# Performance work log

Measured on AMD Instinct MI355X. Metric: run time of the kernel, lower is better.

The kernel has to match this reference:

```python
import jax, jax.numpy as jnp
import numpy as np

B, N, D = 16, 32768, 256
OUT = 256
TOP_K = 64


def setup_inputs() -> dict:
    key = jax.random.key(0)
    ks = jax.random.split(key, 10)
    s = 0.02
    return {
        "tem_emb": jax.random.normal(ks[0], (B, N, D), dtype=jnp.float32),
        "year": 1,
        "init_hidden": jax.random.normal(ks[1], (D, 1), dtype=jnp.float32) * s,
        "mlp_w": jax.random.normal(ks[2], (OUT, TOP_K * D), dtype=jnp.float32) * s,
        "mlp_b": jnp.zeros((OUT,), dtype=jnp.float32),
        "Wr_w": jax.random.normal(ks[3], (OUT, 2 * OUT), dtype=jnp.float32) * s,
        "Wr_b": jnp.zeros((OUT,), dtype=jnp.float32),
        "Wz_w": jax.random.normal(ks[4], (OUT, 2 * OUT), dtype=jnp.float32) * s,
        "Wz_b": jnp.zeros((OUT,), dtype=jnp.float32),
        "Wt_w": jax.random.normal(ks[5], (OUT, 2 * OUT), dtype=jnp.float32) * s,
        "Wt_b": jnp.zeros((OUT,), dtype=jnp.float32),
    }


def reference(tem_emb, year, init_hidden, mlp_w, mlp_b, Wr_w, Wr_b, Wz_w, Wz_b, Wt_w, Wt_b):
    b, n, d = tem_emb.shape
    x = jnp.swapaxes(tem_emb, 1, 2)              # [B, D, N]
    h0 = init_hidden[:, 0]                        # [D]; no prev year -> init_hidden branch
    prev = h0[None, :, None]                      # broadcasts to [B, D, N]

    # select_k=True: abs-diff top-k over N, per (B, D) row
    diff = jnp.abs(x - prev)                      # [B, D, N]
    _, top_idx = jax.lax.top_k(diff, TOP_K)       # [B, D, K]
    feats = jnp.take_along_axis(x, top_idx, axis=2)  # [B, D, K]
    flat = feats.reshape(b, d * TOP_K)            # [B, D*K]
    ts_in = flat @ mlp_w.T + mlp_b                # [B, OUT]

    # is_update=True: GatedUpdateCell(ts_in, mean_N(prev_hidden))
    h_prev = jnp.broadcast_to(h0, (b, d))         # mean over N of constant broadcast
    comb = jnp.concatenate([ts_in, h_prev], axis=-1)          # [B, 2*OUT]
    r = jax.nn.sigmoid(comb @ Wr_w.T + Wr_b)
    z = jax.nn.sigmoid(comb @ Wz_w.T + Wz_b)
    comb2 = jnp.concatenate([ts_in, h_prev * r], axis=-1)
    h_t = jnp.tanh(comb2 @ Wt_w.T + Wt_b)
    h_next = z * h_t + (1.0 - z) * ts_in          # [B, OUT]

    return jnp.broadcast_to(h_next[:, :, None], (b, OUT, n))  # [B, OUT, N]
```

## Files before the change

### kernel.cpp

```cpp
#include <hip/hip_runtime.h>
#include <stdint.h>

#define BB 16
#define NN 32768
#define DD 256
#define OUTD 256
#define TOPK 64
#define NTASK (BB * DD)
#define THRESH 2.75f
#define CAPMAX 512

typedef unsigned long long u64;
typedef unsigned int u32;

__device__ __forceinline__ u64 make_key(float diff, int n) {
    union { float f; u32 i; } c; c.f = diff;
    return ((u64)c.i << 15) | (u64)(u32)(32767 - n);
}

__global__ __launch_bounds__(256) void k_scan(const float4* __restrict__ t4,
                                              const float* __restrict__ h0,
                                              u32* __restrict__ cnt,
                                              u64* __restrict__ surv,
                                              int cap) {
    __shared__ float h0s[DD];
    h0s[threadIdx.x] = h0[threadIdx.x];
    __syncthreads();
    const int total = (BB * NN * DD) / 4;
    for (int v = blockIdx.x * blockDim.x + threadIdx.x; v < total; v += gridDim.x * blockDim.x) {
        float4 w = t4[v];
        int d0 = (v & 63) << 2;
        int n  = (v >> 6) & (NN - 1);
        int b  = v >> 21;
        float xs[4] = {w.x, w.y, w.z, w.w};
#pragma unroll
        for (int q = 0; q < 4; ++q) {
            float df = fabsf(xs[q] - h0s[d0 + q]);
            if (df >= THRESH) {
                int task = (b << 8) + d0 + q;
                u32 pos = atomicAdd(&cnt[task], 1u);
                if ((int)pos < cap)
                    surv[(size_t)task * cap + pos] = make_key(df, n);
            }
        }
    }
}

__global__ __launch_bounds__(64) void k_select(const u32* __restrict__ cnt,
                                               const u64* __restrict__ surv,
                                               const float* __restrict__ tem,
                                               float* __restrict__ feats, int cap) {
    int task = blockIdx.x;
    int c = (int)cnt[task];
    if (c < TOPK || c > cap) return;
    __shared__ u64 keys[CAPMAX];
    for (int i = threadIdx.x; i < CAPMAX; i += 64)
        keys[i] = (i < c) ? surv[(size_t)task * cap + i] : 0ull;
    __syncthreads();
    for (int k = 2; k <= CAPMAX; k <<= 1) {
        for (int j = k >> 1; j > 0; j >>= 1) {
            for (int i = threadIdx.x; i < CAPMAX; i += 64) {
                int ixj = i ^ j;
                if (ixj > i) {
                    u64 a = keys[i], bb = keys[ixj];
                    bool up = ((i & k) == 0);
                    if (up ? (a < bb) : (a > bb)) { keys[i] = bb; keys[ixj] = a; }
                }
            }
            __syncthreads();
        }
    }
    if (threadIdx.x < TOPK) {
        int n = 32767 - (int)(keys[threadIdx.x] & 0x7FFFu);
        int b = task >> 8, d = task & 255;
        feats[task * TOPK + threadIdx.x] = tem[((size_t)b * NN + n) * DD + d];
    }
}

__global__ __launch_bounds__(64) void k_fallback(const float* __restrict__ tem,
                                                 const float* __restrict__ h0,
                                                 const u32* __restrict__ cnt,
                                                 float* __restrict__ feats, int cap) {
    int task = blockIdx.x;
    int c = (int)cnt[task];
    if (c >= TOPK && c <= cap) return;
    int b = task >> 8, d = task & 255;
    float h = h0[d];
    int lane = threadIdx.x;
    const float* base = tem + (size_t)b * NN * DD + d;
    u64 prev = ~0ull;
    for (int k = 0; k < TOPK; ++k) {
        u64 best = 0ull;
        for (int n = lane; n < NN; n += 64) {
            float df = fabsf(base[(size_t)n * DD] - h);
            u64 key = make_key(df, n);
            if (key < prev && key > best) best = key;
        }
        for (int off = 32; off > 0; off >>= 1) {
            u64 o = __shfl_xor(best, off, 64);
            if (o > best) best = o;
        }
        if (lane == 0) {
            int n = 32767 - (int)(best & 0x7FFFu);
            feats[task * TOPK + k] = base[(size_t)n * DD];
        }
        prev = best;
    }
}

__global__ __launch_bounds__(256) void k_mlp(const float* __restrict__ mlp_w,
                                             const float* __restrict__ feats,
                                             float* __restrict__ ts_raw) {
    int Wv = blockIdx.x * 4 + (threadIdx.x >> 6);
    int lane = threadIdx.x & 63;
    int o = Wv >> 4, b = Wv & 15;
    const float4* w4 = (const float4*)(mlp_w + (size_t)o * (DD * TOPK));
    const float4* f4 = (const float4*)(feats + b * (DD * TOPK));
    float acc = 0.f;
    for (int j = lane; j < (DD * TOPK) / 4; j += 64) {
        float4 wv = w4[j]; float4 fv = f4[j];
        acc += wv.x * fv.x + wv.y * fv.y + wv.z * fv.z + wv.w * fv.w;
    }
    for (int off = 32; off > 0; off >>= 1) acc += __shfl_down(acc, off, 64);
    if (lane == 0) ts_raw[b * OUTD + o] = acc;
}

__global__ __launch_bounds__(256) void k_gru(const float* __restrict__ ts_raw,
                                             const float* __restrict__ mlp_b,
                                             const float* __restrict__ h0,
                                             const float* __restrict__ Wr_w,
                                             const float* __restrict__ Wr_b,
                                             const float* __restrict__ Wz_w,
                                             const float* __restrict__ Wz_b,
                                             const float* __restrict__ Wt_w,
                                             const float* __restrict__ Wt_b,
                                             float* __restrict__ h_next) {
    int b = blockIdx.x, o = threadIdx.x;
    __shared__ float comb[2 * OUTD];
    __shared__ float rh[OUTD];
    float ts = ts_raw[b * OUTD + o] + mlp_b[o];
    float h = h0[o];
    comb[o] = ts; comb[OUTD + o] = h;
    __syncthreads();
    const float4* wr = (const float4*)(Wr_w + (size_t)o * 2 * OUTD);
    const float4* wz = (const float4*)(Wz_w + (size_t)o * 2 * OUTD);
    float ar = Wr_b[o], az = Wz_b[o];
    for (int j = 0; j < (2 * OUTD) / 4; ++j) {
        float4 a = wr[j];
        ar += a.x * comb[4 * j] + a.y * comb[4 * j + 1] + a.z * comb[4 * j + 2] + a.w * comb[4 * j + 3];
        float4 c = wz[j];
        az += c.x * comb[4 * j] + c.y * comb[4 * j + 1] + c.z * comb[4 * j + 2] + c.w * comb[4 * j + 3];
    }
    float r = 1.f / (1.f + expf(-ar));
    float z = 1.f / (1.f + expf(-az));
    rh[o] = h * r;
    __syncthreads();
    const float4* wt = (const float4*)(Wt_w + (size_t)o * 2 * OUTD);
    float at = Wt_b[o];
    for (int j = 0; j < OUTD / 4; ++j) {
        float4 a = wt[j];
        at += a.x * comb[4 * j] + a.y * comb[4 * j + 1] + a.z * comb[4 * j + 2] + a.w * comb[4 * j + 3];
    }
    for (int j = 0; j < OUTD / 4; ++j) {
        float4 a = wt[OUTD / 4 + j];
        at += a.x * rh[4 * j] + a.y * rh[4 * j + 1] + a.z * rh[4 * j + 2] + a.w * rh[4 * j + 3];
    }
    float ht = tanhf(at);
    h_next[b * OUTD + o] = z * ht + (1.f - z) * ts;
}

__global__ __launch_bounds__(256) void k_bcast(const float* __restrict__ h_next,
                                               float4* __restrict__ out) {
    const int total = (BB * OUTD * NN) / 4;
    for (int v = blockIdx.x * blockDim.x + threadIdx.x; v < total; v += gridDim.x * blockDim.x) {
        int row = v >> 13;
        float h = h_next[row];
        out[v] = make_float4(h, h, h, h);
    }
}

extern "C" void kernel_launch(void* const* d_in, const int* in_sizes, int n_in,
                              void* d_out, int out_size, void* d_ws, size_t ws_size,
                              hipStream_t stream) {
    const float* tem   = (const float*)d_in[0];
    const float* h0    = (const float*)d_in[2];
    const float* mlp_w = (const float*)d_in[3];
    const float* mlp_b = (const float*)d_in[4];
    const float* Wr_w  = (const float*)d_in[5];
    const float* Wr_b  = (const float*)d_in[6];
    const float* Wz_w  = (const float*)d_in[7];
    const float* Wz_b  = (const float*)d_in[8];
    const float* Wt_w  = (const float*)d_in[9];
    const float* Wt_b  = (const float*)d_in[10];

    char* ws = (char*)d_ws;
    u32* cnt      = (u32*)ws;
    float* ts_raw = (float*)(ws + 16384);
    float* h_next = (float*)(ws + 32768);
    float* feats  = (float*)(ws + 49152);
    const size_t surv_off = 49152 + 1048576;
    u64* surv = (u64*)(ws + surv_off);
    int cap = 0;
    if (ws_size > surv_off) {
        size_t avail = (ws_size - surv_off) / ((size_t)NTASK * 8);
        cap = (int)(avail > CAPMAX ? CAPMAX : avail);
    }

    hipMemsetAsync(cnt, 0, NTASK * sizeof(u32), stream);
    k_scan<<<8192, 256, 0, stream>>>((const float4*)tem, h0, cnt, surv, cap);
    k_select<<<NTASK, 64, 0, stream>>>(cnt, surv, tem, feats, cap);
    k_fallback<<<NTASK, 64, 0, stream>>>(tem, h0, cnt, feats, cap);
    k_mlp<<<1024, 256, 0, stream>>>(mlp_w, feats, ts_raw);
    k_gru<<<BB, 256, 0, stream>>>(ts_raw, mlp_b, h0, Wr_w, Wr_b, Wz_w, Wz_b, Wt_w, Wt_b, h_next);
    k_bcast<<<8192, 256, 0, stream>>>(h_next, (float4*)d_out);
}
```

Measured before the change: 1.094 ms.

## Replace bitonic sort with rank counting, merge fallback, share MLP weight loads

```diff
diff --git a/kernel.cpp b/kernel.cpp
--- a/kernel.cpp
+++ b/kernel.cpp
@@ -46,83 +46,81 @@
     }
 }
 
-__global__ __launch_bounds__(64) void k_select(const u32* __restrict__ cnt,
-                                               const u64* __restrict__ surv,
-                                               const float* __restrict__ tem,
-                                               float* __restrict__ feats, int cap) {
+__global__ __launch_bounds__(128) void k_select(const u32* __restrict__ cnt,
+                                                const u64* __restrict__ surv,
+                                                const float* __restrict__ tem,
+                                                const float* __restrict__ h0,
+                                                float* __restrict__ feats, int cap) {
     int task = blockIdx.x;
     int c = (int)cnt[task];
-    if (c < TOPK || c > cap) return;
-    __shared__ u64 keys[CAPMAX];
-    for (int i = threadIdx.x; i < CAPMAX; i += 64)
-        keys[i] = (i < c) ? surv[(size_t)task * cap + i] : 0ull;
-    __syncthreads();
-    for (int k = 2; k <= CAPMAX; k <<= 1) {
-        for (int j = k >> 1; j > 0; j >>= 1) {
-            for (int i = threadIdx.x; i < CAPMAX; i += 64) {
-                int ixj = i ^ j;
-                if (ixj > i) {
-                    u64 a = keys[i], bb = keys[ixj];
-                    bool up = ((i & k) == 0);
-                    if (up ? (a < bb) : (a > bb)) { keys[i] = bb; keys[ixj] = a; }
-                }
-            }
-            __syncthreads();
+    int b = task >> 8, d = task & 255;
+    if (c >= TOPK && c <= cap) {
+        __shared__ u64 keys[CAPMAX];
+        for (int i = threadIdx.x; i < c; i += 128)
+            keys[i] = surv[(size_t)task * cap + i];
+        __syncthreads();
+        for (int i = threadIdx.x; i < c; i += 128) {
+            u64 me = keys[i];
+            int rank = 0;
+#pragma unroll 4
+            for (int j = 0; j < c; ++j)
+                rank += (keys[j] > me) ? 1 : 0;
+            if (rank < TOPK) {
+                int n = 32767 - (int)(me & 0x7FFFu);
+                feats[task * TOPK + rank] = tem[((size_t)b * NN + n) * DD + d];
+            }
         }
-    }
-    if (threadIdx.x < TOPK) {
-        int n = 32767 - (int)(keys[threadIdx.x] & 0x7FFFu);
-        int b = task >> 8, d = task & 255;
-        feats[task * TOPK + threadIdx.x] = tem[((size_t)b * NN + n) * DD + d];
-    }
-}
-
-__global__ __launch_bounds__(64) void k_fallback(const float* __restrict__ tem,
-                                                 const float* __restrict__ h0,
-                                                 const u32* __restrict__ cnt,
-                                                 float* __restrict__ feats, int cap) {
-    int task = blockIdx.x;
-    int c = (int)cnt[task];
-    if (c >= TOPK && c <= cap) return;
-    int b = task >> 8, d = task & 255;
-    float h = h0[d];
-    int lane = threadIdx.x;
-    const float* base = tem + (size_t)b * NN * DD + d;
-    u64 prev = ~0ull;
-    for (int k = 0; k < TOPK; ++k) {
-        u64 best = 0ull;
-        for (int n = lane; n < NN; n += 64) {
-            float df = fabsf(base[(size_t)n * DD] - h);
-            u64 key = make_key(df, n);
-            if (key < prev && key > best) best = key;
+    } else {
+        if (threadIdx.x >= 64) return;
+        int lane = threadIdx.x;
+        float h = h0[d];
+        const float* base = tem + (size_t)b * NN * DD + d;
+        u64 prev = ~0ull;
+        for (int k = 0; k < TOPK; ++k) {
+            u64 best = 0ull;
+            for (int n = lane; n < NN; n += 64) {
+                float df = fabsf(base[(size_t)n * DD] - h);
+                u64 key = make_key(df, n);
+                if (key < prev && key > best) best = key;
+            }
+            for (int off = 32; off > 0; off >>= 1) {
+                u64 o = __shfl_xor(best, off, 64);
+                if (o > best) best = o;
+            }
+            if (lane == 0) {
+                int n = 32767 - (int)(best & 0x7FFFu);
+                feats[task * TOPK + k] = base[(size_t)n * DD];
+            }
+            prev = best;
         }
-        for (int off = 32; off > 0; off >>= 1) {
-            u64 o = __shfl_xor(best, off, 64);
-            if (o > best) best = o;
-        }
-        if (lane == 0) {
-            int n = 32767 - (int)(best & 0x7FFFu);
-            feats[task * TOPK + k] = base[(size_t)n * DD];
-        }
-        prev = best;
-    }
-}
-
-__global__ __launch_bounds__(256) void k_mlp(const float* __restrict__ mlp_w,
+    }
+}
+
+__global__ __launch_bounds__(512) void k_mlp(const float* __restrict__ mlp_w,
                                              const float* __restrict__ feats,
                                              float* __restrict__ ts_raw) {
-    int Wv = blockIdx.x * 4 + (threadIdx.x >> 6);
-    int lane = threadIdx.x & 63;
-    int o = Wv >> 4, b = Wv & 15;
+    int o = blockIdx.x;
+    int wv = threadIdx.x >> 6, lane = threadIdx.x & 63;
+    int b0 = wv, b1 = wv + 8;
     const float4* w4 = (const float4*)(mlp_w + (size_t)o * (DD * TOPK));
-    const float4* f4 = (const float4*)(feats + b * (DD * TOPK));
-    float acc = 0.f;
+    const float4* f0 = (const float4*)(feats + b0 * (DD * TOPK));
+    const float4* f1 = (const float4*)(feats + b1 * (DD * TOPK));
+    float a0 = 0.f, a1 = 0.f;
     for (int j = lane; j < (DD * TOPK) / 4; j += 64) {
-        float4 wv = w4[j]; float4 fv = f4[j];
-        acc += wv.x * fv.x + wv.y * fv.y + wv.z * fv.z + wv.w * fv.w;
-    }
-    for (int off = 32; off > 0; off >>= 1) acc += __shfl_down(acc, off, 64);
-    if (lane == 0) ts_raw[b * OUTD + o] = acc;
+        float4 wvv = w4[j];
+        float4 x0 = f0[j];
+        float4 x1 = f1[j];
+        a0 += wvv.x * x0.x + wvv.y * x0.y + wvv.z * x0.z + wvv.w * x0.w;
+        a1 += wvv.x * x1.x + wvv.y * x1.y + wvv.z * x1.z + wvv.w * x1.w;
+    }
+    for (int off = 32; off > 0; off >>= 1) {
+        a0 += __shfl_down(a0, off, 64);
+        a1 += __shfl_down(a1, off, 64);
+    }
+    if (lane == 0) {
+        ts_raw[b0 * OUTD + o] = a0;
+        ts_raw[b1 * OUTD + o] = a1;
+    }
 }
 
 __global__ __launch_bounds__(256) void k_gru(const float* __restrict__ ts_raw,
@@ -208,9 +206,8 @@
 
     hipMemsetAsync(cnt, 0, NTASK * sizeof(u32), stream);
     k_scan<<<8192, 256, 0, stream>>>((const float4*)tem, h0, cnt, surv, cap);
-    k_select<<<NTASK, 64, 0, stream>>>(cnt, surv, tem, feats, cap);
-    k_fallback<<<NTASK, 64, 0, stream>>>(tem, h0, cnt, feats, cap);
-    k_mlp<<<1024, 256, 0, stream>>>(mlp_w, feats, ts_raw);
+    k_select<<<NTASK, 128, 0, stream>>>(cnt, surv, tem, h0, feats, cap);
+    k_mlp<<<OUTD, 512, 0, stream>>>(mlp_w, feats, ts_raw);
     k_gru<<<BB, 256, 0, stream>>>(ts_raw, mlp_b, h0, Wr_w, Wr_b, Wz_w, Wz_b, Wt_w, Wt_b, h_next);
     k_bcast<<<8192, 256, 0, stream>>>(h_next, (float4*)d_out);
 }
```

Result: faster. 1.049 ms (-4.2%).
